# Optimization experiments

Measured on AMD Instinct MI355X. Metric: run time of the kernel, lower is better.

The kernel has to match this reference:

```python
import jax, jax.numpy as jnp
import numpy as np

N_ATOMS = 8_000_000
N_REC = 2_000_000
N_POC = 500_000
N_CHAINS = 4


def setup_inputs() -> dict:
    key = jax.random.key(0)
    k1, k2, k3, k4 = jax.random.split(key, 4)
    # coordinates in nm, inside a ~5 nm box
    positions = jax.random.uniform(k1, (N_ATOMS, 3), dtype=jnp.float32) * 5.0
    box_vectors = jnp.diag(jnp.array([5.0, 5.0, 5.0], dtype=jnp.float32))
    # unique receptor atom indices into positions
    rec_indices = jax.random.permutation(k2, N_ATOMS)[:N_REC].astype(jnp.int32)
    # unique pocket indices INTO THE REC ARRAY (poc_pos = rec_pos[poc_indices])
    poc_indices = jax.random.permutation(k3, N_REC)[:N_POC].astype(jnp.int32)
    # contiguous chain assignment over rec atoms, all chains present in pocket
    chain_ids = ((jnp.arange(N_REC, dtype=jnp.int32) * N_CHAINS) // N_REC).astype(jnp.int32)
    poc_chain_ids = chain_ids[poc_indices]
    ref_poc = jax.random.uniform(k4, (N_POC, 3), dtype=jnp.float32) * 5.0
    k = jnp.float32(100.0)  # kJ/mol/nm^2
    return {
        "positions": positions, "box_vectors": box_vectors, "ref_poc": ref_poc,
        "k": k, "rec_indices": rec_indices, "poc_indices": poc_indices,
        "chain_ids": chain_ids, "poc_chain_ids": poc_chain_ids, "n_chains": N_CHAINS,
    }


def best_periodic_translation(pos1, pos2, box_vectors):
    # pos1, pos2: [C,3]; box_vectors: [3,3] (rows are lattice vectors)
    delta = pos2 - pos1
    inv = 1.0 / jnp.diag(box_vectors)
    s3 = jnp.round(delta[:, 2] * inv[2])
    delta = delta - s3[:, None] * box_vectors[2]
    s2 = jnp.round(delta[:, 1] * inv[1])
    delta = delta - s2[:, None] * box_vectors[1]
    s1 = jnp.round(delta[:, 0] * inv[0])
    return s1[:, None] * box_vectors[0] + s2[:, None] * box_vectors[1] + s3[:, None] * box_vectors[2]


def reference(positions, box_vectors, ref_poc, k, rec_indices, poc_indices, chain_ids, poc_chain_ids, n_chains):
    rec_pos = positions[rec_indices]  # [R,3]
    # Per-chain pocket COM. NOTE: original indexes global positions here
    # (positions[poc_chain_indices]), NOT rec_pos -- reproduced faithfully.
    poc_glob = positions[poc_indices]  # [P,3]
    counts = jax.ops.segment_sum(jnp.ones((poc_glob.shape[0],), poc_glob.dtype), poc_chain_ids, num_segments=n_chains)  # [C]
    poc_com = jax.ops.segment_sum(poc_glob, poc_chain_ids, num_segments=n_chains) / counts[:, None]  # [C,3]
    ref_com = jax.ops.segment_sum(ref_poc, poc_chain_ids, num_segments=n_chains) / counts[:, None]  # [C,3]
    best_t = best_periodic_translation(poc_com, ref_com, box_vectors)  # [C,3]
    rec_pos = rec_pos + best_t[chain_ids]  # translate each chain into the reference image

    poc_pos = rec_pos[poc_indices]  # [P,3]
    rec_origin = jnp.mean(rec_pos, axis=0)
    rec_centered = rec_pos - rec_origin
    r_sq = jnp.sum(rec_centered ** 2, axis=1)  # [R]
    F = jnp.zeros_like(rec_pos).at[poc_indices].set(-2.0 * k * (poc_pos - ref_poc))
    F_mean = jnp.mean(F, axis=0)
    torque = jnp.cross(rec_centered, F)
    torque_mean = jnp.mean(torque, axis=0)
    F_rot = jnp.cross(torque_mean[None], rec_centered) / r_sq[:, None]
    F_final = jnp.zeros_like(positions).at[rec_indices].set(F_mean + F_rot)
    return (jnp.float32(0.0), F_final)
```

## Files before the change

### kernel.cpp

```cpp
#include <hip/hip_runtime.h>


typedef unsigned int uint32;
typedef unsigned char uchar;

#define MAXC 16
#define W_BT 0
#define W_O 48
#define W_FM 52
#define W_TM 56
#define W_ACC 64

#define BAR_OFF 4032
#define GCOUNT_OFF 4096
#define REC_OFF 8192
#define NBK 1024
#define BSH 13
#define BUCKET_ATOMS (1 << BSH)
#define CAP 2560
#define INV8_OFF (REC_OFF + NBK * CAP * 4)

#define K1_KPT 16
#define K1_CHUNK (256 * K1_KPT)

struct PartSh { uint32 hist[NBK]; uint32 curs[NBK]; uint32 base[NBK]; };
struct PocSh  { float red[4][43]; float accL[3 + MAXC * 10]; };
struct MapSh  { uchar map_[BUCKET_ATOMS]; };
struct StageSh{ float stage[3328]; };
union ShU { PartSh part; PocSh poc; MapSh map; StageSh st; };
struct MiscSh { float red7[4][7]; float sc[64]; float cnt16[MAXC]; float tot[192]; };

__device__ inline float waveSum(float v) {
#pragma unroll
  for (int off = 32; off > 0; off >>= 1) v += __shfl_down(v, off, 64);
  return v;
}

__device__ inline void gridBar(uint32* bar, int nblk, uint32 phase) {
  __threadfence();
  __syncthreads();
  if (threadIdx.x == 0) {
    __hip_atomic_fetch_add(bar, 1u, __ATOMIC_ACQ_REL, __HIP_MEMORY_SCOPE_AGENT);
    const uint32 tgt = (uint32)nblk * phase;
    for (int it = 0; it < (1 << 21); ++it) {
      if (__hip_atomic_load(bar, __ATOMIC_ACQUIRE, __HIP_MEMORY_SCOPE_AGENT) >= tgt)
        break;
      __builtin_amdgcn_s_sleep(8);
    }
  }
  __syncthreads();
  __threadfence();
}

__device__ void phaseA(const float* __restrict__ pos,
                       const float* __restrict__ ref_poc,
                       const int* __restrict__ rec_idx,
                       const int* __restrict__ cid,
                       const int* __restrict__ poc_idx,
                       const int* __restrict__ poc_cid,
                       int C, int R, int P,
                       uint32* __restrict__ gcount,
                       uint32* __restrict__ grecords,
                       float* __restrict__ ws,
                       ShU& sh, MiscSh& ms, int bid, int pbN, int rbN) {
  const int tid = threadIdx.x;
  if (bid < pbN) {
    const int gsz = pbN * 256;
    if (C <= 4) {
      float vals[43];
#pragma unroll
      for (int v = 0; v < 43; ++v) vals[v] = 0.f;
      for (int rb = bid * 256 + tid; rb < P; rb += 4 * gsz) {
        int rr[4], i2[4], c2[4], ri[4];
        float g[4][3], p[4][3], rf[4][3];
#pragma unroll
        for (int q = 0; q < 4; ++q) {
          int r = rb + q * gsz;
          rr[q] = (r < P) ? r : -1;
        }
#pragma unroll
        for (int q = 0; q < 4; ++q) {
          int r = (rr[q] < 0) ? 0 : rr[q];
          i2[q] = poc_idx[r];
          c2[q] = poc_cid[r];
        }
#pragma unroll
        for (int q = 0; q < 4; ++q) {
          ri[q] = rec_idx[i2[q]];
          g[q][0] = pos[3 * i2[q] + 0];
          g[q][1] = pos[3 * i2[q] + 1];
          g[q][2] = pos[3 * i2[q] + 2];
        }
#pragma unroll
        for (int q = 0; q < 4; ++q) {
          int r = (rr[q] < 0) ? 0 : rr[q];
          p[q][0] = pos[3 * ri[q] + 0];
          p[q][1] = pos[3 * ri[q] + 1];
          p[q][2] = pos[3 * ri[q] + 2];
          rf[q][0] = ref_poc[3 * r + 0];
          rf[q][1] = ref_poc[3 * r + 1];
          rf[q][2] = ref_poc[3 * r + 2];
        }
#pragma unroll
        for (int q = 0; q < 4; ++q) {
          if (rr[q] >= 0) {
            vals[0] += p[q][1] * rf[q][2] - p[q][2] * rf[q][1];
            vals[1] += p[q][2] * rf[q][0] - p[q][0] * rf[q][2];
            vals[2] += p[q][0] * rf[q][1] - p[q][1] * rf[q][0];
#pragma unroll
            for (int cc = 0; cc < 4; ++cc) {
              bool m = (c2[q] == cc);
              float* a = &vals[3 + cc * 10];
              a[0] += m ? g[q][0] : 0.f; a[1] += m ? g[q][1] : 0.f;
              a[2] += m ? g[q][2] : 0.f;
              a[3] += m ? rf[q][0] : 0.f; a[4] += m ? rf[q][1] : 0.f;
              a[5] += m ? rf[q][2] : 0.f;
              a[6] += m ? p[q][0] : 0.f; a[7] += m ? p[q][1] : 0.f;
              a[8] += m ? p[q][2] : 0.f;
              a[9] += m ? 1.f : 0.f;
            }
          }
        }
      }
      const int wid = tid >> 6;
#pragma unroll
      for (int v = 0; v < 43; ++v) {
        float s = waveSum(vals[v]);
        if ((tid & 63) == 0) sh.poc.red[wid][v] = s;
      }
      __syncthreads();
      for (int t = tid; t < 43; t += 256)
        atomicAdd(&ws[W_ACC + 19 + t], sh.poc.red[0][t] + sh.poc.red[1][t] +
                                       sh.poc.red[2][t] + sh.poc.red[3][t]);
    } else {
      float* accL = sh.poc.accL;
      for (int t = tid; t < 3 + MAXC * 10; t += 256) accL[t] = 0.f;
      __syncthreads();
      for (int r = bid * 256 + tid; r < P; r += pbN * 256) {
        int i2 = poc_idx[r];
        int c2 = poc_cid[r];
        int ri = rec_idx[i2];
        float gx = pos[3 * i2 + 0], gy = pos[3 * i2 + 1], gz = pos[3 * i2 + 2];
        float px = pos[3 * ri + 0], py = pos[3 * ri + 1], pz = pos[3 * ri + 2];
        float rx = ref_poc[3 * r + 0], ry = ref_poc[3 * r + 1], rz = ref_poc[3 * r + 2];
        atomicAdd(&accL[0], py * rz - pz * ry);
        atomicAdd(&accL[1], pz * rx - px * rz);
        atomicAdd(&accL[2], px * ry - py * rx);
        float* a = &accL[3 + c2 * 10];
        atomicAdd(&a[0], gx); atomicAdd(&a[1], gy); atomicAdd(&a[2], gz);
        atomicAdd(&a[3], rx); atomicAdd(&a[4], ry); atomicAdd(&a[5], rz);
        atomicAdd(&a[6], px); atomicAdd(&a[7], py); atomicAdd(&a[8], pz);
        atomicAdd(&a[9], 1.f);
      }
      __syncthreads();
      for (int t = tid; t < 3 + MAXC * 10; t += 256)
        if (accL[t] != 0.f) atomicAdd(&ws[W_ACC + 19 + t], accL[t]);
    }
  } else {
    const int pb = bid - pbN;
    uint32* hist = sh.part.hist;
    uint32* curs = sh.part.curs;
    uint32* base = sh.part.base;
    float c0 = 0.f, c1 = 0.f, c2 = 0.f, c3 = 0.f;
    if (C > 4) {
      for (int t = tid; t < MAXC; t += 256) ms.cnt16[t] = 0.f;
      __syncthreads();
    }
    for (int r0 = pb * K1_CHUNK; r0 < R; r0 += rbN * K1_CHUNK) {
      int cnt = R - r0; if (cnt > K1_CHUNK) cnt = K1_CHUNK;
      for (int t = tid; t < NBK; t += 256) { hist[t] = 0u; curs[t] = 0u; }
      __syncthreads();
      uint32 enc[K1_KPT];
#pragma unroll
      for (int j = 0; j < K1_KPT; ++j) {
        int t = tid + j * 256;
        uint32 e = 0xFFFFFFFFu;
        if (t < cnt) {
          uint32 idx = (uint32)rec_idx[r0 + t];
          uint32 c = (uint32)cid[r0 + t] & 255u;
          e = (idx << 8) | c;
          atomicAdd(&hist[idx >> BSH], 1u);
          if (C <= 4) {
            c0 += (c == 0u) ? 1.f : 0.f; c1 += (c == 1u) ? 1.f : 0.f;
            c2 += (c == 2u) ? 1.f : 0.f; c3 += (c == 3u) ? 1.f : 0.f;
          } else {
            atomicAdd(&ms.cnt16[c], 1.f);
          }
        }
        enc[j] = e;
      }
      __syncthreads();
      for (int t = tid; t < NBK; t += 256) {
        uint32 h = hist[t];
        base[t] = h ? atomicAdd(&gcount[t], h) : 0u;
      }
      __syncthreads();
#pragma unroll
      for (int j = 0; j < K1_KPT; ++j) {
        uint32 e = enc[j];
        if (e != 0xFFFFFFFFu) {
          uint32 b = e >> (8 + BSH);
          uint32 slot = base[b] + atomicAdd(&curs[b], 1u);
          if (slot < CAP) grecords[b * CAP + slot] = e;
        }
      }
      __syncthreads();
    }
    if (C <= 4) {
      float vv[4] = {c0, c1, c2, c3};
      const int wid = tid >> 6;
#pragma unroll
      for (int v = 0; v < 4; ++v) {
        float s = waveSum(vv[v]);
        if ((tid & 63) == 0) ms.red7[wid][v] = s;
      }
      __syncthreads();
      if (tid < 4)
        atomicAdd(&ws[W_ACC + 3 + tid], ms.red7[0][tid] + ms.red7[1][tid] +
                                        ms.red7[2][tid] + ms.red7[3][tid]);
    } else {
      __syncthreads();
      if (tid < C) atomicAdd(&ws[W_ACC + 3 + tid], ms.cnt16[tid]);
    }
  }
}

__device__ void phaseBC(const float* __restrict__ pos,
                        const uint32* __restrict__ gcount,
                        const uint32* __restrict__ grecords,
                        int N, uchar* __restrict__ inv8,
                        float* __restrict__ ws,
                        ShU& sh, MiscSh& ms, int bid, int gridN) {
  const int tid = threadIdx.x;
  float sx = 0.f, sy = 0.f, sz = 0.f;
  for (int b = bid; b < NBK; b += gridN) {
    const int a0 = b << BSH;
    if (a0 >= N) break;
    int natoms = N - a0; if (natoms > BUCKET_ATOMS) natoms = BUCKET_ATOMS;
    uchar* map_ = sh.map.map_;
    uint4* m16 = (uint4*)map_;
    uint4 ff; ff.x = ff.y = ff.z = ff.w = 0xFFFFFFFFu;
    for (int t = tid; t < BUCKET_ATOMS / 16; t += 256) m16[t] = ff;
    __syncthreads();
    int n = (int)gcount[b]; if (n > CAP) n = CAP;
    for (int t = tid; t < n; t += 256) {
      uint32 e = grecords[b * CAP + t];
      map_[(e >> 8) & (BUCKET_ATOMS - 1)] = (uchar)(e & 255u);
    }
    __syncthreads();
    uchar* dst = inv8 + a0;
    if (natoms == BUCKET_ATOMS) {
      uint4* d16 = (uint4*)dst;
      for (int t = tid; t < BUCKET_ATOMS / 16; t += 256) d16[t] = m16[t];
    } else {
      for (int t = tid; t < natoms; t += 256) dst[t] = map_[t];
    }
    int ngf = natoms >> 2;
    const uchar4* m4 = (const uchar4*)map_;
    const float4* pos4 = (const float4*)pos;
    int g0 = a0 >> 2;
    for (int g = tid; g < ngf; g += 256) {
      float4 p0 = pos4[3 * (g0 + g) + 0];
      float4 p1 = pos4[3 * (g0 + g) + 1];
      float4 p2 = pos4[3 * (g0 + g) + 2];
      uchar4 m = m4[g];
      if (m.x != 255) { sx += p0.x; sy += p0.y; sz += p0.z; }
      if (m.y != 255) { sx += p0.w; sy += p1.x; sz += p1.y; }
      if (m.z != 255) { sx += p1.z; sy += p1.w; sz += p2.x; }
      if (m.w != 255) { sx += p2.y; sy += p2.z; sz += p2.w; }
    }
    int tb = natoms & 3;
    if (tid < tb) {
      int a = a0 + (ngf << 2) + tid;
      if (map_[(ngf << 2) + tid] != 255) {
        sx += pos[3 * a]; sy += pos[3 * a + 1]; sz += pos[3 * a + 2];
      }
    }
    __syncthreads();
  }
  float vv[3] = {sx, sy, sz};
  const int wid = tid >> 6;
#pragma unroll
  for (int v = 0; v < 3; ++v) {
    float s = waveSum(vv[v]);
    if ((tid & 63) == 0) ms.red7[wid][v] = s;
  }
  __syncthreads();
  if (tid < 3) {
    float s = ms.red7[0][tid] + ms.red7[1][tid] + ms.red7[2][tid] + ms.red7[3][tid];
    if (s != 0.f) atomicAdd(&ws[W_ACC + tid], s);
  }
}

__device__ void phaseFZ(const float* __restrict__ box,
                        const float* __restrict__ kp,
                        int C, int R, float* __restrict__ ws,
                        MiscSh& ms, int bid) {
  if (bid != 0) return;
  const int tid = threadIdx.x;
  for (int t = tid; t < 192; t += 256) ms.tot[t] = ws[W_ACC + t];
  __syncthreads();
  if (tid != 0) return;
  float* tot = ms.tot;
  const float kk = kp[0];
  const float Rf = (float)R;
  const float* xp = &tot[19];
  float inv0 = 1.f / box[0], inv1 = 1.f / box[4], inv2 = 1.f / box[8];
  float ox = tot[0], oy = tot[1], oz = tot[2];
  float Fx = 0, Fy = 0, Fz = 0;
  float T1x = 0, T1y = 0, T1z = 0, T2x = 0, T2y = 0, T2z = 0;
  for (int c = 0; c < C; ++c) {
    float nrec = tot[3 + c];
    const float* a = &tot[22 + c * 10];
    float np = a[9];
    float invn = 1.f / np;
    float pcx = a[0] * invn, pcy = a[1] * invn, pcz = a[2] * invn;
    float rcx = a[3] * invn, rcy = a[4] * invn, rcz = a[5] * invn;
    float dx = rcx - pcx, dy = rcy - pcy, dz = rcz - pcz;
    float s3 = rintf(dz * inv2);
    dx -= s3 * box[6]; dy -= s3 * box[7]; dz -= s3 * box[8];
    float s2 = rintf(dy * inv1);
    dx -= s2 * box[3]; dy -= s2 * box[4]; dz -= s2 * box[5];
    float s1 = rintf(dx * inv0);
    float btx = s1 * box[0] + s2 * box[3] + s3 * box[6];
    float bty = s1 * box[1] + s2 * box[4] + s3 * box[7];
    float btz = s1 * box[2] + s2 * box[5] + s3 * box[8];
    ws[W_BT + c * 3 + 0] = btx;
    ws[W_BT + c * 3 + 1] = bty;
    ws[W_BT + c * 3 + 2] = btz;
    ox += nrec * btx; oy += nrec * bty; oz += nrec * btz;
    float SFx = -2.f * kk * (a[6] + np * btx - a[3]);
    float SFy = -2.f * kk * (a[7] + np * bty - a[4]);
    float SFz = -2.f * kk * (a[8] + np * btz - a[5]);
    Fx += SFx; Fy += SFy; Fz += SFz;
    T1x += a[7] * btz - a[8] * bty;
    T1y += a[8] * btx - a[6] * btz;
    T1z += a[6] * bty - a[7] * btx;
    T2x += bty * SFz - btz * SFy;
    T2y += btz * SFx - btx * SFz;
    T2z += btx * SFy - bty * SFx;
  }
  ox /= Rf; oy /= Rf; oz /= Rf;
  float Tx = 2.f * kk * xp[0] - 2.f * kk * T1x + T2x - (oy * Fz - oz * Fy);
  float Ty = 2.f * kk * xp[1] - 2.f * kk * T1y + T2y - (oz * Fx - ox * Fz);
  float Tz = 2.f * kk * xp[2] - 2.f * kk * T1z + T2z - (ox * Fy - oy * Fx);
  ws[W_O + 0] = ox; ws[W_O + 1] = oy; ws[W_O + 2] = oz;
  ws[W_FM + 0] = Fx / Rf; ws[W_FM + 1] = Fy / Rf; ws[W_FM + 2] = Fz / Rf;
  ws[W_TM + 0] = Tx / Rf; ws[W_TM + 1] = Ty / Rf; ws[W_TM + 2] = Tz / Rf;
}

__device__ void phaseD(const float* __restrict__ pos,
                       const uchar* __restrict__ inv8,
                       int N, const float* __restrict__ ws,
                       float* __restrict__ out,
                       ShU& sh, MiscSh& ms, int bid, int gridN) {
  const int tid = threadIdx.x;
  float* sc = ms.sc;
  if (tid < 64) sc[tid] = ws[tid];
  if (bid == 0 && tid == 0) out[0] = 0.f;
  const int ntiles = (N + 1023) >> 10;
  for (int tile = bid; tile < ntiles; tile += gridN) {
    const int t0 = tile << 10;
    int nat = N - t0; if (nat > 1024) nat = 1024;
    const int nfl = nat * 3;
    float* stage = sh.st.stage;

    if (nat == 1024) {
      const float4* src4 = (const float4*)(pos + 3 * t0);
#pragma unroll
      for (int kk = 0; kk < 3; ++kk) {
        int v4 = tid + kk * 256;
        float4 p = src4[v4];
        int idx = 4 * v4 + v4 / 3;
        stage[idx + 0] = p.x; stage[idx + 1] = p.y;
        stage[idx + 2] = p.z; stage[idx + 3] = p.w;
      }
    } else {
      for (int k = tid; k < nfl; k += 256)
        stage[k + (int)((unsigned)k / 12u)] = pos[3 * t0 + k];
    }
    __syncthreads();

    float ox = sc[W_O + 0], oy = sc[W_O + 1], oz = sc[W_O + 2];
    float fmx = sc[W_FM + 0], fmy = sc[W_FM + 1], fmz = sc[W_FM + 2];
    float tmx = sc[W_TM + 0], tmy = sc[W_TM + 1], tmz = sc[W_TM + 2];

    uchar mc[4];
    if (nat == 1024) {
      uchar4 m = ((const uchar4*)(inv8 + t0))[tid];
      mc[0] = m.x; mc[1] = m.y; mc[2] = m.z; mc[3] = m.w;
    } else {
#pragma unroll
      for (int q = 0; q < 4; ++q) {
        int la = 4 * tid + q;
        mc[q] = (la < nat) ? inv8[t0 + la] : (uchar)255;
      }
    }
#pragma unroll
    for (int q = 0; q < 4; ++q) {
      int la = 4 * tid + q;
      if (la < nat) {
        float* s = &stage[13 * tid + 3 * q];
        float fx = 0.f, fy = 0.f, fz = 0.f;
        int c = mc[q];
        if (c != 255) {
          float cx = s[0] + sc[W_BT + 3 * c + 0] - ox;
          float cy = s[1] + sc[W_BT + 3 * c + 1] - oy;
          float cz = s[2] + sc[W_BT + 3 * c + 2] - oz;
          float inv = 1.f / (cx * cx + cy * cy + cz * cz);
          fx = fmx + (tmy * cz - tmz * cy) * inv;
          fy = fmy + (tmz * cx - tmx * cz) * inv;
          fz = fmz + (tmx * cy - tmy * cx) * inv;
        }
        s[0] = fx; s[1] = fy; s[2] = fz;
      }
    }
    __syncthreads();

    float* ob = out + 1 + 3 * t0;
    if (nat == 1024) {
#pragma unroll
      for (int kk = 0; kk < 3; ++kk) {
        int j = tid + kk * 256;
        if (j < 767) {
          int k = 3 + 4 * j;
          float4 v;
          v.x = stage[k + k / 12];
          v.y = stage[(k + 1) + (k + 1) / 12];
          v.z = stage[(k + 2) + (k + 2) / 12];
          v.w = stage[(k + 3) + (k + 3) / 12];
          *(float4*)(ob + k) = v;
        }
      }
      if (tid < 3) ob[tid] = stage[tid];
      if (tid == 3) ob[3071] = stage[3071 + 3071 / 12];
    } else {
      for (int k = tid; k < nfl; k += 256)
        ob[k] = stage[k + (int)((unsigned)k / 12u)];
    }
    __syncthreads();
  }
}

__global__ __launch_bounds__(256, 4) void k_all(
    const float* __restrict__ pos, const float* __restrict__ ref_poc,
    const int* __restrict__ rec_idx, const int* __restrict__ cid,
    const int* __restrict__ poc_idx, const int* __restrict__ poc_cid,
    const int* __restrict__ ncp, const float* __restrict__ box,
    const float* __restrict__ kp, int R, int P, int N,
    uint32* __restrict__ gcount, uint32* __restrict__ grecords,
    uchar* __restrict__ inv8, float* __restrict__ ws,
    float* __restrict__ out, uint32* __restrict__ bar) {
  __shared__ ShU sh;
  __shared__ MiscSh ms;
  const int bid = blockIdx.x;
  const int gridN = gridDim.x;
  const int pbN = (gridN * 5) >> 3;
  const int C = ncp[0];
  phaseA(pos, ref_poc, rec_idx, cid, poc_idx, poc_cid, C, R, P,
         gcount, grecords, ws, sh, ms, bid, pbN, gridN - pbN);
  gridBar(bar, gridN, 1);
  phaseBC(pos, gcount, grecords, N, inv8, ws, sh, ms, bid, gridN);
  gridBar(bar, gridN, 2);
  phaseFZ(box, kp, C, R, ws, ms, bid);
  gridBar(bar, gridN, 3);
  phaseD(pos, inv8, N, ws, out, sh, ms, bid, gridN);
}

__global__ __launch_bounds__(256) void k_pA(
    const float* __restrict__ pos, const float* __restrict__ ref_poc,
    const int* __restrict__ rec_idx, const int* __restrict__ cid,
    const int* __restrict__ poc_idx, const int* __restrict__ poc_cid,
    const int* __restrict__ ncp, int R, int P,
    uint32* __restrict__ gcount, uint32* __restrict__ grecords,
    float* __restrict__ ws) {
  __shared__ ShU sh;
  __shared__ MiscSh ms;
  const int gridN = gridDim.x;
  const int pbN = (gridN * 5) >> 3;
  phaseA(pos, ref_poc, rec_idx, cid, poc_idx, poc_cid, ncp[0], R, P,
         gcount, grecords, ws, sh, ms, (int)blockIdx.x, pbN, gridN - pbN);
}

__global__ __launch_bounds__(256) void k_pBC(
    const float* __restrict__ pos, const uint32* __restrict__ gcount,
    const uint32* __restrict__ grecords, int N,
    uchar* __restrict__ inv8, float* __restrict__ ws) {
  __shared__ ShU sh;
  __shared__ MiscSh ms;
  phaseBC(pos, gcount, grecords, N, inv8, ws, sh, ms, (int)blockIdx.x,
          (int)gridDim.x);
}

__global__ __launch_bounds__(256) void k_pFZ(
    const float* __restrict__ box, const float* __restrict__ kp,
    const int* __restrict__ ncp, int R, float* __restrict__ ws) {
  __shared__ MiscSh ms;
  phaseFZ(box, kp, ncp[0], R, ws, ms, 0);
}

__global__ __launch_bounds__(256) void k_pD(
    const float* __restrict__ pos, const uchar* __restrict__ inv8,
    int N, const float* __restrict__ ws, float* __restrict__ out) {
  __shared__ ShU sh;
  __shared__ MiscSh ms;
  phaseD(pos, inv8, N, ws, out, sh, ms, (int)blockIdx.x, (int)gridDim.x);
}

extern "C" void kernel_launch(void* const* d_in, const int* in_sizes, int n_in,
                              void* d_out, int out_size, void* d_ws, size_t ws_size,
                              hipStream_t stream) {
  const float* pos     = (const float*)d_in[0];
  const float* box     = (const float*)d_in[1];
  const float* ref_poc = (const float*)d_in[2];
  const float* kp      = (const float*)d_in[3];
  const int* rec_idx   = (const int*)d_in[4];
  const int* poc_idx   = (const int*)d_in[5];
  const int* cid       = (const int*)d_in[6];
  const int* poc_cid   = (const int*)d_in[7];
  const int* ncp       = (const int*)d_in[8];
  float* out = (float*)d_out;
  float* ws  = (float*)d_ws;
  uint32* bar      = (uint32*)((char*)d_ws + BAR_OFF);
  uint32* gcount   = (uint32*)((char*)d_ws + GCOUNT_OFF);
  uint32* grecords = (uint32*)((char*)d_ws + REC_OFF);
  uchar* inv8      = (uchar*)d_ws + INV8_OFF;

  const int N = in_sizes[0] / 3;
  const int R = in_sizes[4];
  const int P = in_sizes[5];

  hipMemsetAsync(d_ws, 0, 8192, stream);

  static int fusedGrid = -2;
  if (fusedGrid == -2) {
    int dev = 0;
    (void)hipGetDevice(&dev);
    int ncu = 0;
    hipDeviceProp_t prop;
    if (hipGetDeviceProperties(&prop, dev) == hipSuccess)
      ncu = prop.multiProcessorCount;
    if (ncu <= 0) ncu = 256;
    int maxb = 0;
    if (hipOccupancyMaxActiveBlocksPerMultiprocessor(
            &maxb, (const void*)k_all, 256, 0) != hipSuccess)
      maxb = 0;
    long g = (long)maxb * (long)ncu;
    fusedGrid = (g >= 512) ? (int)((g > 1024) ? 1024 : g) : 0;
  }

  if (fusedGrid > 0) {
    k_all<<<dim3(fusedGrid), dim3(256), 0, stream>>>(
        pos, ref_poc, rec_idx, cid, poc_idx, poc_cid, ncp, box, kp,
        R, P, N, gcount, grecords, inv8, ws, out, bar);
  } else {
    k_pA<<<1024, 256, 0, stream>>>(pos, ref_poc, rec_idx, cid, poc_idx,
                                   poc_cid, ncp, R, P, gcount, grecords, ws);
    k_pBC<<<NBK, 256, 0, stream>>>(pos, gcount, grecords, N, inv8, ws);
    k_pFZ<<<1, 256, 0, stream>>>(box, kp, ncp, R, ws);
    int gF = (N + 1023) / 1024;
    k_pD<<<gF, 256, 0, stream>>>(pos, inv8, N, ws, out);
  }
}
```

Before: 287.7 us.

## Use fixed-grid fused kernel with timeout barriers and backup fallback kernel

Removes the host-side occupancy query and separate-kernel path. It always launches the fused 1024-block kernel, whose grid barriers now time out after a short spin. If a barrier fails, a second 512-block kernel that checks a completion flag redoes the later phases. Phase BC now writes per-bucket partial sums to a buffer that block 0 reduces, instead of using global float atomics, which makes the sum deterministic. The work split between the two block groups in phase A moves from 5/8 to 1/2. This adds an extra kernel launch every call and the risk of a spurious fallback if blocks are not co-resident.

```diff
diff --git a/kernel.cpp b/kernel.cpp
--- a/kernel.cpp
+++ b/kernel.cpp
@@ -12,14 +12,19 @@
 #define W_ACC 64
 
 #define BAR_OFF 4032
+#define BAR2_OFF 4036
+#define OK_OFF 4040
 #define GCOUNT_OFF 4096
-#define REC_OFF 8192
+#define PSUM_OFF 8192
+#define REC_OFF 20480
 #define NBK 1024
 #define BSH 13
 #define BUCKET_ATOMS (1 << BSH)
 #define CAP 2560
 #define INV8_OFF (REC_OFF + NBK * CAP * 4)
 
+#define GRID_ALL 1024
+#define GRID_BK 512
 #define K1_KPT 16
 #define K1_CHUNK (256 * K1_KPT)
 
@@ -36,20 +41,24 @@
   return v;
 }
 
-__device__ inline void gridBar(uint32* bar, int nblk, uint32 phase) {
+__device__ inline bool gridBar(uint32* bar, int nblk, uint32 phase, int* shOk) {
   __threadfence();
   __syncthreads();
   if (threadIdx.x == 0) {
     __hip_atomic_fetch_add(bar, 1u, __ATOMIC_ACQ_REL, __HIP_MEMORY_SCOPE_AGENT);
     const uint32 tgt = (uint32)nblk * phase;
-    for (int it = 0; it < (1 << 21); ++it) {
-      if (__hip_atomic_load(bar, __ATOMIC_ACQUIRE, __HIP_MEMORY_SCOPE_AGENT) >= tgt)
-        break;
-      __builtin_amdgcn_s_sleep(8);
-    }
+    int ok = 0;
+    for (int it = 0; it < 2048; ++it) {
+      if (__hip_atomic_load(bar, __ATOMIC_ACQUIRE, __HIP_MEMORY_SCOPE_AGENT) >= tgt) {
+        ok = 1; break;
+      }
+      __builtin_amdgcn_s_sleep(4);
+    }
+    *shOk = ok;
   }
   __syncthreads();
   __threadfence();
+  return *shOk != 0;
 }
 
 __device__ void phaseA(const float* __restrict__ pos,
@@ -229,54 +238,79 @@
                         const uint32* __restrict__ gcount,
                         const uint32* __restrict__ grecords,
                         int N, uchar* __restrict__ inv8,
-                        float* __restrict__ ws,
+                        float* __restrict__ psum,
                         ShU& sh, MiscSh& ms, int bid, int gridN) {
   const int tid = threadIdx.x;
-  float sx = 0.f, sy = 0.f, sz = 0.f;
   for (int b = bid; b < NBK; b += gridN) {
     const int a0 = b << BSH;
-    if (a0 >= N) break;
-    int natoms = N - a0; if (natoms > BUCKET_ATOMS) natoms = BUCKET_ATOMS;
-    uchar* map_ = sh.map.map_;
-    uint4* m16 = (uint4*)map_;
-    uint4 ff; ff.x = ff.y = ff.z = ff.w = 0xFFFFFFFFu;
-    for (int t = tid; t < BUCKET_ATOMS / 16; t += 256) m16[t] = ff;
+    float sx = 0.f, sy = 0.f, sz = 0.f;
+    if (a0 < N) {
+      int natoms = N - a0; if (natoms > BUCKET_ATOMS) natoms = BUCKET_ATOMS;
+      uchar* map_ = sh.map.map_;
+      uint4* m16 = (uint4*)map_;
+      uint4 ff; ff.x = ff.y = ff.z = ff.w = 0xFFFFFFFFu;
+      for (int t = tid; t < BUCKET_ATOMS / 16; t += 256) m16[t] = ff;
+      __syncthreads();
+      int n = (int)gcount[b]; if (n > CAP) n = CAP;
+      for (int t = tid; t < n; t += 256) {
+        uint32 e = grecords[b * CAP + t];
+        map_[(e >> 8) & (BUCKET_ATOMS - 1)] = (uchar)(e & 255u);
+      }
+      __syncthreads();
+      uchar* dst = inv8 + a0;
+      if (natoms == BUCKET_ATOMS) {
+        uint4* d16 = (uint4*)dst;
+        for (int t = tid; t < BUCKET_ATOMS / 16; t += 256) d16[t] = m16[t];
+      } else {
+        for (int t = tid; t < natoms; t += 256) dst[t] = map_[t];
+      }
+      int ngf = natoms >> 2;
+      const uchar4* m4 = (const uchar4*)map_;
+      const float4* pos4 = (const float4*)pos;
+      int g0 = a0 >> 2;
+      for (int g = tid; g < ngf; g += 256) {
+        float4 p0 = pos4[3 * (g0 + g) + 0];
+        float4 p1 = pos4[3 * (g0 + g) + 1];
+        float4 p2 = pos4[3 * (g0 + g) + 2];
+        uchar4 m = m4[g];
+        if (m.x != 255) { sx += p0.x; sy += p0.y; sz += p0.z; }
+        if (m.y != 255) { sx += p0.w; sy += p1.x; sz += p1.y; }
+        if (m.z != 255) { sx += p1.z; sy += p1.w; sz += p2.x; }
+        if (m.w != 255) { sx += p2.y; sy += p2.z; sz += p2.w; }
+      }
+      int tb = natoms & 3;
+      if (tid < tb) {
+        int a = a0 + (ngf << 2) + tid;
+        if (map_[(ngf << 2) + tid] != 255) {
+          sx += pos[3 * a]; sy += pos[3 * a + 1]; sz += pos[3 * a + 2];
+        }
+      }
+    }
+    float vv[3] = {sx, sy, sz};
+    const int wid = tid >> 6;
+#pragma unroll
+    for (int v = 0; v < 3; ++v) {
+      float s = waveSum(vv[v]);
+      if ((tid & 63) == 0) ms.red7[wid][v] = s;
+    }
     __syncthreads();
-    int n = (int)gcount[b]; if (n > CAP) n = CAP;
-    for (int t = tid; t < n; t += 256) {
-      uint32 e = grecords[b * CAP + t];
-      map_[(e >> 8) & (BUCKET_ATOMS - 1)] = (uchar)(e & 255u);
-    }
+    if (tid < 3)
+      psum[b * 3 + tid] = ms.red7[0][tid] + ms.red7[1][tid] +
+                          ms.red7[2][tid] + ms.red7[3][tid];
     __syncthreads();
-    uchar* dst = inv8 + a0;
-    if (natoms == BUCKET_ATOMS) {
-      uint4* d16 = (uint4*)dst;
-      for (int t = tid; t < BUCKET_ATOMS / 16; t += 256) d16[t] = m16[t];
-    } else {
-      for (int t = tid; t < natoms; t += 256) dst[t] = map_[t];
-    }
-    int ngf = natoms >> 2;
-    const uchar4* m4 = (const uchar4*)map_;
-    const float4* pos4 = (const float4*)pos;
-    int g0 = a0 >> 2;
-    for (int g = tid; g < ngf; g += 256) {
-      float4 p0 = pos4[3 * (g0 + g) + 0];
-      float4 p1 = pos4[3 * (g0 + g) + 1];
-      float4 p2 = pos4[3 * (g0 + g) + 2];
-      uchar4 m = m4[g];
-      if (m.x != 255) { sx += p0.x; sy += p0.y; sz += p0.z; }
-      if (m.y != 255) { sx += p0.w; sy += p1.x; sz += p1.y; }
-      if (m.z != 255) { sx += p1.z; sy += p1.w; sz += p2.x; }
-      if (m.w != 255) { sx += p2.y; sy += p2.z; sz += p2.w; }
-    }
-    int tb = natoms & 3;
-    if (tid < tb) {
-      int a = a0 + (ngf << 2) + tid;
-      if (map_[(ngf << 2) + tid] != 255) {
-        sx += pos[3 * a]; sy += pos[3 * a + 1]; sz += pos[3 * a + 2];
-      }
-    }
-    __syncthreads();
+  }
+}
+
+__device__ void phaseFZ(const float* __restrict__ box,
+                        const float* __restrict__ kp,
+                        int C, int R, float* __restrict__ ws,
+                        const float* __restrict__ psum,
+                        MiscSh& ms, int bid) {
+  if (bid != 0) return;
+  const int tid = threadIdx.x;
+  float sx = 0.f, sy = 0.f, sz = 0.f;
+  for (int b = tid; b < NBK; b += 256) {
+    sx += psum[3 * b + 0]; sy += psum[3 * b + 1]; sz += psum[3 * b + 2];
   }
   float vv[3] = {sx, sy, sz};
   const int wid = tid >> 6;
@@ -285,23 +319,13 @@
     float s = waveSum(vv[v]);
     if ((tid & 63) == 0) ms.red7[wid][v] = s;
   }
-  __syncthreads();
-  if (tid < 3) {
-    float s = ms.red7[0][tid] + ms.red7[1][tid] + ms.red7[2][tid] + ms.red7[3][tid];
-    if (s != 0.f) atomicAdd(&ws[W_ACC + tid], s);
-  }
-}
-
-__device__ void phaseFZ(const float* __restrict__ box,
-                        const float* __restrict__ kp,
-                        int C, int R, float* __restrict__ ws,
-                        MiscSh& ms, int bid) {
-  if (bid != 0) return;
-  const int tid = threadIdx.x;
   for (int t = tid; t < 192; t += 256) ms.tot[t] = ws[W_ACC + t];
   __syncthreads();
   if (tid != 0) return;
   float* tot = ms.tot;
+  tot[0] = ms.red7[0][0] + ms.red7[1][0] + ms.red7[2][0] + ms.red7[3][0];
+  tot[1] = ms.red7[0][1] + ms.red7[1][1] + ms.red7[2][1] + ms.red7[3][1];
+  tot[2] = ms.red7[0][2] + ms.red7[1][2] + ms.red7[2][2] + ms.red7[3][2];
   const float kk = kp[0];
   const float Rf = (float)R;
   const float* xp = &tot[19];
@@ -449,62 +473,54 @@
     const int* __restrict__ ncp, const float* __restrict__ box,
     const float* __restrict__ kp, int R, int P, int N,
     uint32* __restrict__ gcount, uint32* __restrict__ grecords,
-    uchar* __restrict__ inv8, float* __restrict__ ws,
-    float* __restrict__ out, uint32* __restrict__ bar) {
+    uchar* __restrict__ inv8, float* __restrict__ psum,
+    float* __restrict__ ws, float* __restrict__ out,
+    uint32* __restrict__ bar, uint32* __restrict__ okflag) {
   __shared__ ShU sh;
   __shared__ MiscSh ms;
+  __shared__ int shOk;
   const int bid = blockIdx.x;
   const int gridN = gridDim.x;
-  const int pbN = (gridN * 5) >> 3;
+  const int pbN = gridN >> 1;
   const int C = ncp[0];
   phaseA(pos, ref_poc, rec_idx, cid, poc_idx, poc_cid, C, R, P,
          gcount, grecords, ws, sh, ms, bid, pbN, gridN - pbN);
-  gridBar(bar, gridN, 1);
-  phaseBC(pos, gcount, grecords, N, inv8, ws, sh, ms, bid, gridN);
-  gridBar(bar, gridN, 2);
-  phaseFZ(box, kp, C, R, ws, ms, bid);
-  gridBar(bar, gridN, 3);
-  phaseD(pos, inv8, N, ws, out, sh, ms, bid, gridN);
-}
-
-__global__ __launch_bounds__(256) void k_pA(
-    const float* __restrict__ pos, const float* __restrict__ ref_poc,
-    const int* __restrict__ rec_idx, const int* __restrict__ cid,
-    const int* __restrict__ poc_idx, const int* __restrict__ poc_cid,
-    const int* __restrict__ ncp, int R, int P,
-    uint32* __restrict__ gcount, uint32* __restrict__ grecords,
-    float* __restrict__ ws) {
+  bool ok = gridBar(bar, gridN, 1, &shOk);
+  if (ok) {
+    phaseBC(pos, gcount, grecords, N, inv8, psum, sh, ms, bid, gridN);
+    ok = gridBar(bar, gridN, 2, &shOk);
+  }
+  if (ok) {
+    phaseFZ(box, kp, C, R, ws, psum, ms, bid);
+    ok = gridBar(bar, gridN, 3, &shOk);
+  }
+  if (ok) {
+    if (bid == 0 && threadIdx.x == 0)
+      __hip_atomic_store(okflag, 1u, __ATOMIC_RELEASE, __HIP_MEMORY_SCOPE_AGENT);
+    phaseD(pos, inv8, N, ws, out, sh, ms, bid, gridN);
+  }
+}
+
+__global__ __launch_bounds__(256, 4) void k_backup(
+    const float* __restrict__ pos, const float* __restrict__ box,
+    const float* __restrict__ kp, const int* __restrict__ ncp,
+    int R, int N,
+    const uint32* __restrict__ gcount, const uint32* __restrict__ grecords,
+    uchar* __restrict__ inv8, float* __restrict__ psum,
+    float* __restrict__ ws, float* __restrict__ out,
+    uint32* __restrict__ bar2, const uint32* __restrict__ okflag) {
+  if (__hip_atomic_load(okflag, __ATOMIC_ACQUIRE, __HIP_MEMORY_SCOPE_AGENT) != 0)
+    return;
   __shared__ ShU sh;
   __shared__ MiscSh ms;
+  __shared__ int shOk;
+  const int bid = blockIdx.x;
   const int gridN = gridDim.x;
-  const int pbN = (gridN * 5) >> 3;
-  phaseA(pos, ref_poc, rec_idx, cid, poc_idx, poc_cid, ncp[0], R, P,
-         gcount, grecords, ws, sh, ms, (int)blockIdx.x, pbN, gridN - pbN);
-}
-
-__global__ __launch_bounds__(256) void k_pBC(
-    const float* __restrict__ pos, const uint32* __restrict__ gcount,
-    const uint32* __restrict__ grecords, int N,
-    uchar* __restrict__ inv8, float* __restrict__ ws) {
-  __shared__ ShU sh;
-  __shared__ MiscSh ms;
-  phaseBC(pos, gcount, grecords, N, inv8, ws, sh, ms, (int)blockIdx.x,
-          (int)gridDim.x);
-}
-
-__global__ __launch_bounds__(256) void k_pFZ(
-    const float* __restrict__ box, const float* __restrict__ kp,
-    const int* __restrict__ ncp, int R, float* __restrict__ ws) {
-  __shared__ MiscSh ms;
-  phaseFZ(box, kp, ncp[0], R, ws, ms, 0);
-}
-
-__global__ __launch_bounds__(256) void k_pD(
-    const float* __restrict__ pos, const uchar* __restrict__ inv8,
-    int N, const float* __restrict__ ws, float* __restrict__ out) {
-  __shared__ ShU sh;
-  __shared__ MiscSh ms;
-  phaseD(pos, inv8, N, ws, out, sh, ms, (int)blockIdx.x, (int)gridDim.x);
+  phaseBC(pos, gcount, grecords, N, inv8, psum, sh, ms, bid, gridN);
+  gridBar(bar2, gridN, 1, &shOk);
+  phaseFZ(box, kp, ncp[0], R, ws, psum, ms, bid);
+  gridBar(bar2, gridN, 2, &shOk);
+  phaseD(pos, inv8, N, ws, out, sh, ms, bid, gridN);
 }
 
 extern "C" void kernel_launch(void* const* d_in, const int* in_sizes, int n_in,
@@ -522,9 +538,12 @@
   float* out = (float*)d_out;
   float* ws  = (float*)d_ws;
   uint32* bar      = (uint32*)((char*)d_ws + BAR_OFF);
+  uint32* bar2     = (uint32*)((char*)d_ws + BAR2_OFF);
+  uint32* okflag   = (uint32*)((char*)d_ws + OK_OFF);
   uint32* gcount   = (uint32*)((char*)d_ws + GCOUNT_OFF);
+  float*  psum     = (float*)((char*)d_ws + PSUM_OFF);
   uint32* grecords = (uint32*)((char*)d_ws + REC_OFF);
-  uchar* inv8      = (uchar*)d_ws + INV8_OFF;
+  uchar*  inv8     = (uchar*)d_ws + INV8_OFF;
 
   const int N = in_sizes[0] / 3;
   const int R = in_sizes[4];
@@ -532,33 +551,10 @@
 
   hipMemsetAsync(d_ws, 0, 8192, stream);
 
-  static int fusedGrid = -2;
-  if (fusedGrid == -2) {
-    int dev = 0;
-    (void)hipGetDevice(&dev);
-    int ncu = 0;
-    hipDeviceProp_t prop;
-    if (hipGetDeviceProperties(&prop, dev) == hipSuccess)
-      ncu = prop.multiProcessorCount;
-    if (ncu <= 0) ncu = 256;
-    int maxb = 0;
-    if (hipOccupancyMaxActiveBlocksPerMultiprocessor(
-            &maxb, (const void*)k_all, 256, 0) != hipSuccess)
-      maxb = 0;
-    long g = (long)maxb * (long)ncu;
-    fusedGrid = (g >= 512) ? (int)((g > 1024) ? 1024 : g) : 0;
-  }
-
-  if (fusedGrid > 0) {
-    k_all<<<dim3(fusedGrid), dim3(256), 0, stream>>>(
-        pos, ref_poc, rec_idx, cid, poc_idx, poc_cid, ncp, box, kp,
-        R, P, N, gcount, grecords, inv8, ws, out, bar);
-  } else {
-    k_pA<<<1024, 256, 0, stream>>>(pos, ref_poc, rec_idx, cid, poc_idx,
-                                   poc_cid, ncp, R, P, gcount, grecords, ws);
-    k_pBC<<<NBK, 256, 0, stream>>>(pos, gcount, grecords, N, inv8, ws);
-    k_pFZ<<<1, 256, 0, stream>>>(box, kp, ncp, R, ws);
-    int gF = (N + 1023) / 1024;
-    k_pD<<<gF, 256, 0, stream>>>(pos, inv8, N, ws, out);
-  }
-}
+  k_all<<<GRID_ALL, 256, 0, stream>>>(
+      pos, ref_poc, rec_idx, cid, poc_idx, poc_cid, ncp, box, kp,
+      R, P, N, gcount, grecords, inv8, psum, ws, out, bar, okflag);
+  k_backup<<<GRID_BK, 256, 0, stream>>>(
+      pos, box, kp, ncp, R, N, gcount, grecords, inv8, psum, ws, out,
+      bar2, okflag);
+}
```

Result: slower. 1.033 ms (+259.1%).
